# Performance work log

Hardware: AMD Instinct MI355X
Metric: run time of the kernel (lower is better)

The kernel has to match this reference:

```python
import jax, jax.numpy as jnp
import numpy as np

B, C, H, W = 8, 256, 64, 64
NH = 8
CM = 2048
EPS = 1e-5


def setup_inputs() -> dict:
    key = jax.random.key(0)
    ks = jax.random.split(key, 16)
    n = lambda k, s: (jax.random.normal(k, s, dtype=jnp.float32) * 0.02)
    return {
        'x': jax.random.normal(ks[0], (B, C, H, W), dtype=jnp.float32),
        'Wqkv': n(ks[1], (C, 3 * C)), 'bqkv': n(ks[2], (3 * C,)),
        'dw_w': n(ks[3], (C, 1, 3, 3)), 'dw_b': n(ks[4], (C,)),
        'Wproj': n(ks[5], (C, C)), 'bproj': n(ks[6], (C,)),
        'bn1_g': jnp.ones((C,), jnp.float32), 'bn1_b': jnp.zeros((C,), jnp.float32),
        'bn1_m': n(ks[7], (C,)), 'bn1_v': jax.random.uniform(ks[8], (C,), dtype=jnp.float32) + 0.5,
        'alpha1': jnp.ones((1,), jnp.float32),
        'Wfc1': n(ks[9], (C, CM)), 'bfc1': n(ks[10], (CM,)),
        'Wfc2': n(ks[11], (CM, C)), 'bfc2': n(ks[12], (C,)),
        'bn2_g': jnp.ones((C,), jnp.float32), 'bn2_b': jnp.zeros((C,), jnp.float32),
        'bn2_m': n(ks[13], (C,)), 'bn2_v': jax.random.uniform(ks[14], (C,), dtype=jnp.float32) + 0.5,
        'alpha2': jnp.ones((1,), jnp.float32),
    }


def _repbn(x, g, b, m, v, alpha):
    # eval-mode RepBN: BatchNorm1d with running stats over channel dim + alpha*x
    bn = (x - m) * jax.lax.rsqrt(v + EPS) * g + b
    return bn + alpha * x


def reference(x, Wqkv, bqkv, dw_w, dw_b, Wproj, bproj,
              bn1_g, bn1_b, bn1_m, bn1_v, alpha1,
              Wfc1, bfc1, Wfc2, bfc2,
              bn2_g, bn2_b, bn2_m, bn2_v, alpha2):
    b, c, h, w = x.shape
    n = h * w
    hd = c // NH
    scale = hd ** (-0.5)
    t = x.reshape(b, c, n).transpose(0, 2, 1)  # [B,N,C]

    # --- SimplifiedLinearAttention ---
    qkv = (t @ Wqkv + bqkv).reshape(b, n, 3, NH, hd).transpose(2, 0, 3, 1, 4)
    q, k, v = qkv[0], qkv[1], qkv[2]          # [B,H,N,hd]
    q = jax.nn.relu(q) * scale
    k = jax.nn.relu(k)
    ctx = jnp.einsum('bhnd,bhne->bhde', k, v)  # [B,H,hd,hd] small context
    out = jnp.einsum('bhnd,bhde->bhne', q, ctx)
    out = out.transpose(0, 2, 1, 3).reshape(b, n, c)
    img = out.transpose(0, 2, 1).reshape(b, c, h, w)
    img = jax.lax.conv_general_dilated(img, dw_w, (1, 1), 'SAME',
                                       feature_group_count=c)
    img = img + dw_b[None, :, None, None]
    out = img.reshape(b, c, n).transpose(0, 2, 1)
    out = out @ Wproj + bproj

    # residual + RepBN (eval branch of LinearNorm)
    t = _repbn(t + out, bn1_g, bn1_b, bn1_m, bn1_v, alpha1)

    # FFN (exact GELU as nn.GELU default)
    ff = jax.nn.gelu(t @ Wfc1 + bfc1, approximate=False) @ Wfc2 + bfc2
    t = _repbn(t + ff, bn2_g, bn2_b, bn2_m, bn2_v, alpha2)

    return t.transpose(0, 2, 1).reshape(b, c, h, w)
```

## Files before the change

### kernel.cpp

```cpp
#include <hip/hip_runtime.h>
#include <hip/hip_bf16.h>
#include <math.h>

constexpr int B_ = 8, C_ = 256, H_ = 64, W_ = 64;
constexpr int N_ = H_ * W_;
constexpr int NH_ = 8;
constexpr int CM_ = 2048;
constexpr int M_ = B_ * N_;
constexpr float EPS_ = 1e-5f;

typedef __bf16 bf16_t;
typedef bf16_t bf16x4 __attribute__((ext_vector_type(4)));
typedef bf16_t bf16x8 __attribute__((ext_vector_type(8)));
typedef float f32x4 __attribute__((ext_vector_type(4)));

__device__ inline bf16_t f2b(float f) {
    __hip_bfloat16 h = __float2bfloat16(f);
    return *reinterpret_cast<bf16_t*>(&h);
}
__device__ inline float b2f(bf16_t b) {
    unsigned short u = *reinterpret_cast<unsigned short*>(&b);
    unsigned int x = (unsigned int)u << 16;
    return *reinterpret_cast<float*>(&x);
}
__device__ inline unsigned pk2(float lo, float hi) {
    bf16_t l = f2b(lo), h = f2b(hi);
    unsigned short ls = *reinterpret_cast<unsigned short*>(&l);
    unsigned short hs = *reinterpret_cast<unsigned short*>(&h);
    return ((unsigned)hs << 16) | (unsigned)ls;
}
__device__ inline float gelu_ap(float y) {
    float u = y * (0.7978845608f + 0.0356774081f * y * y);
    float e = __expf(2.0f * u);
    return y - y * __builtin_amdgcn_rcpf(e + 1.0f);
}

#define GLOAD_LDS16(gptr, lptr)                                                     \
    __builtin_amdgcn_global_load_lds(                                               \
        (const __attribute__((address_space(1))) void*)(gptr),                      \
        (__attribute__((address_space(3))) void*)(lptr), 16, 0, 0)

__global__ __launch_bounds__(256)
void prep(const float* __restrict__ x, bf16_t* __restrict__ t_b,
          const float* __restrict__ Wqkv, bf16_t* __restrict__ WqkvT,
          const float* __restrict__ Wproj, bf16_t* __restrict__ WprojT,
          const float* __restrict__ Wfc1, bf16_t* __restrict__ Wfc1T,
          const float* __restrict__ Wfc2, bf16_t* __restrict__ Wfc2T) {
    __shared__ float tile[32][33];
    int id = blockIdx.x;
    int tx = threadIdx.x, ty = threadIdx.y;

    const float* src;
    bf16_t* dst;
    int K, N, k0, n0;

    if (id < 8192) {
        int b = id >> 10, rem = id & 1023;
        int nn = (rem & 127) * 32, cc = (rem >> 7) * 32;
#pragma unroll
        for (int i = ty; i < 32; i += 8)
            tile[i][tx] = x[(size_t)b * C_ * N_ + (size_t)(cc + i) * N_ + nn + tx];
        __syncthreads();
#pragma unroll
        for (int i = ty; i < 32; i += 8)
            t_b[(size_t)b * N_ * C_ + (size_t)(nn + i) * C_ + cc + tx] = f2b(tile[tx][i]);
        return;
    } else if (id < 8384) {
        int idw = id - 8192; K = C_; N = 768;
        n0 = (idw % 24) * 32; k0 = (idw / 24) * 32;
        src = Wqkv; dst = WqkvT;
    } else if (id < 8448) {
        int idw = id - 8384; K = C_; N = C_;
        n0 = (idw & 7) * 32; k0 = (idw >> 3) * 32;
        src = Wproj; dst = WprojT;
    } else if (id < 8960) {
        int idw = id - 8448; K = C_; N = CM_;
        n0 = (idw & 63) * 32; k0 = (idw >> 6) * 32;
        src = Wfc1; dst = Wfc1T;
    } else {
        int idw = id - 8960; K = CM_; N = C_;
        n0 = (idw & 7) * 32; k0 = (idw >> 3) * 32;
        src = Wfc2; dst = Wfc2T;
    }
#pragma unroll
    for (int i = ty; i < 32; i += 8)
        tile[i][tx] = src[(size_t)(k0 + i) * N + n0 + tx];
    __syncthreads();
#pragma unroll
    for (int i = ty; i < 32; i += 8)
        dst[(size_t)(n0 + i) * K + k0 + tx] = f2b(tile[tx][i]);
}

template <int EPI>
__global__ __launch_bounds__(256, 4)
void gemm_swp(const bf16_t* __restrict__ Wt, const bf16_t* __restrict__ Act,
              const float* __restrict__ bias, bf16_t* __restrict__ Cb,
              int M, int N, int K,
              const bf16_t* __restrict__ tres_b,
              const float* __restrict__ g, const float* __restrict__ bb,
              const float* __restrict__ mm, const float* __restrict__ vv,
              const float* __restrict__ alpha) {
    __shared__ bf16x8 ldsv[2048];
    char* lds = (char*)ldsv;

    int tid  = threadIdx.x;
    int lane = tid & 63;
    int w    = tid >> 6;
    int wi   = w >> 1, wj = w & 1;

    int nwg = gridDim.x * gridDim.y;
    int bid = blockIdx.y * gridDim.x + blockIdx.x;
    int swz = (bid & 7) * (nwg >> 3) + (bid >> 3);
    int bx = swz % gridDim.x, by = swz / gridDim.x;
    int bch = bx * 128, bm = by * 128;

    int rowl = lane & 15, kq = lane >> 4;

    f32x4 acc[4][4] = {};

    for (int k0 = 0; k0 < K; k0 += 64) {
#pragma unroll
        for (int j = 0; j < 4; ++j) {
            int jj = w * 4 + j;
            int msub = jj >> 1, kh = jj & 1;
            const bf16_t* gw = Wt + ((size_t)(bch + msub * 16 + rowl) * K + k0 + kh * 32 + kq * 8);
            GLOAD_LDS16(gw, lds + jj * 1024);
            const bf16_t* ga = Act + ((size_t)(bm + msub * 16 + rowl) * K + k0 + kh * 32 + kq * 8);
            GLOAD_LDS16(ga, lds + 16384 + jj * 1024);
        }
        __syncthreads();
#pragma unroll
        for (int ks = 0; ks < 2; ++ks) {
            bf16x8 wf[4], af[4];
#pragma unroll
            for (int i = 0; i < 4; ++i) wf[i] = ldsv[((wi * 4 + i) * 2 + ks) * 64 + lane];
#pragma unroll
            for (int j = 0; j < 4; ++j) af[j] = ldsv[1024 + ((wj * 4 + j) * 2 + ks) * 64 + lane];
#pragma unroll
            for (int i = 0; i < 4; ++i)
#pragma unroll
                for (int j = 0; j < 4; ++j)
                    acc[i][j] = __builtin_amdgcn_mfma_f32_16x16x32_bf16(wf[i], af[j], acc[i][j], 0, 0, 0);
        }
        __syncthreads();
    }

    float alpha_v = (EPI == 1) ? alpha[0] : 0.f;
#pragma unroll
    for (int i = 0; i < 4; ++i) {
        int ch = bch + wi * 64 + i * 16 + (lane >> 4) * 4;
        f32x4 b4 = *(const f32x4*)(bias + ch);
        f32x4 rs4, B4, m4;
        if (EPI == 1) {
            f32x4 g4 = *(const f32x4*)(g + ch);
            f32x4 v4 = *(const f32x4*)(vv + ch);
            B4 = *(const f32x4*)(bb + ch);
            m4 = *(const f32x4*)(mm + ch);
#pragma unroll
            for (int r = 0; r < 4; ++r) rs4[r] = rsqrtf(v4[r] + EPS_) * g4[r];
        }
#pragma unroll
        for (int j = 0; j < 4; ++j) {
            int m = bm + wj * 64 + j * 16 + (lane & 15);
            f32x4 a = acc[i][j];
            bf16_t ob[4];
            if (EPI == 4) {
#pragma unroll
                for (int r = 0; r < 4; ++r) ob[r] = f2b(a[r] + b4[r]);
            } else {
                bf16x4 t4 = *(const bf16x4*)(tres_b + (size_t)m * N + ch);
#pragma unroll
                for (int r = 0; r < 4; ++r) {
                    float z = b2f(t4[r]) + a[r] + b4[r];
                    ob[r] = f2b((z - m4[r]) * rs4[r] + B4[r] + alpha_v * z);
                }
            }
            *(bf16x4*)(Cb + (size_t)m * N + ch) = *(bf16x4*)ob;
        }
    }
}

__global__ __launch_bounds__(512, 4)
void ffn_fused(const bf16_t* __restrict__ Act, const bf16_t* __restrict__ W1t,
               const bf16_t* __restrict__ W2t,
               const float* __restrict__ bfc1, const float* __restrict__ bfc2,
               const float* __restrict__ g, const float* __restrict__ bb,
               const float* __restrict__ mm, const float* __restrict__ vv,
               const float* __restrict__ alpha, float* __restrict__ out) {
    __shared__ char lds[65536];
    bf16x8* ldsA = (bf16x8*)lds;

    const int tid = threadIdx.x;
    const int lane = tid & 63;
    const int w = tid >> 6;
    const int l15 = lane & 15;
    const int kq = lane >> 4;
    const int m0 = blockIdx.x * 64;

#pragma unroll
    for (int j = 0; j < 4; ++j) {
        int jj = w * 4 + j;
        int mblk = jj >> 3, ks = jj & 7;
        const bf16_t* src = Act + (size_t)(m0 + mblk * 16 + l15) * 256 + ks * 32 + kq * 8;
        GLOAD_LDS16(src, lds + jj * 1024);
    }
    __syncthreads();

    f32x4 acc2[2][4] = {};

    const int hrow = w * 16 + l15;
    const int ks2w = w >> 1;
    const int lane2 = l15 + (((2 * w + (kq >> 1)) & 3) << 4);
    const int hwoff = (kq & 1) << 3;
    const int chb = w * 32;

    bf16x8 w1f[8];
#pragma unroll
    for (int ks = 0; ks < 8; ++ks)
        w1f[ks] = *(const bf16x8*)(W1t + (size_t)hrow * 256 + ks * 32 + kq * 8);

    for (int c = 0; c < 16; ++c) {
        f32x4 acc1[4] = {};
#pragma unroll
        for (int ks = 0; ks < 8; ++ks)
#pragma unroll
            for (int mblk = 0; mblk < 4; ++mblk)
                acc1[mblk] = __builtin_amdgcn_mfma_f32_16x16x32_bf16(
                    w1f[ks], ldsA[(mblk * 8 + ks) * 64 + lane], acc1[mblk], 0, 0, 0);

        if (c + 1 < 16) {
#pragma unroll
            for (int ks = 0; ks < 8; ++ks)
                w1f[ks] = *(const bf16x8*)(W1t + (size_t)((c + 1) * 128 + hrow) * 256 + ks * 32 + kq * 8);
        }
        bf16x8 w2f[2][4];
#pragma unroll
        for (int cf = 0; cf < 2; ++cf)
#pragma unroll
            for (int ks2 = 0; ks2 < 4; ++ks2)
                w2f[cf][ks2] = *(const bf16x8*)(W2t + (size_t)(chb + cf * 16 + l15) * 2048 + c * 128 + ks2 * 32 + kq * 8);

        f32x4 b1 = *(const f32x4*)(bfc1 + c * 128 + w * 16 + kq * 4);
        char* hbase = lds + 32768 + (c & 1) * 16384;
#pragma unroll
        for (int mblk = 0; mblk < 4; ++mblk) {
            uint2 u2;
            u2.x = pk2(gelu_ap(acc1[mblk][0] + b1[0]), gelu_ap(acc1[mblk][1] + b1[1]));
            u2.y = pk2(gelu_ap(acc1[mblk][2] + b1[2]), gelu_ap(acc1[mblk][3] + b1[3]));
            *(uint2*)(hbase + (size_t)((mblk * 4 + ks2w) * 64 + lane2) * 16 + hwoff) = u2;
        }
        __syncthreads();

        bf16x8* ldsH = (bf16x8*)(lds + 32768 + (c & 1) * 16384);
#pragma unroll
        for (int mblk = 0; mblk < 4; ++mblk)
#pragma unroll
            for (int ks2 = 0; ks2 < 4; ++ks2) {
                bf16x8 hf = ldsH[(mblk * 4 + ks2) * 64 + lane];
                acc2[0][mblk] = __builtin_amdgcn_mfma_f32_16x16x32_bf16(hf, w2f[0][ks2], acc2[0][mblk], 0, 0, 0);
                acc2[1][mblk] = __builtin_amdgcn_mfma_f32_16x16x32_bf16(hf, w2f[1][ks2], acc2[1][mblk], 0, 0, 0);
            }
    }

    float alpha_v = alpha[0];
#pragma unroll
    for (int cf = 0; cf < 2; ++cf) {
        int ch = chb + cf * 16 + l15;
        float b2v = bfc2[ch];
        float rs = rsqrtf(vv[ch] + EPS_) * g[ch];
        float bbv = bb[ch], mv = mm[ch];
#pragma unroll
        for (int mblk = 0; mblk < 4; ++mblk) {
            int mbase = m0 + mblk * 16 + kq * 4;
            f32x4 o4;
#pragma unroll
            for (int r = 0; r < 4; ++r) {
                float z = b2f(Act[(size_t)(mbase + r) * 256 + ch]) + acc2[cf][mblk][r] + b2v;
                o4[r] = (z - mv) * rs + bbv + alpha_v * z;
            }
            int bi = mbase >> 12, ni = mbase & (N_ - 1);
            *(f32x4*)(out + ((size_t)bi * C_ + ch) * N_ + ni) = o4;
        }
    }
}

__global__ void transpose_b(const bf16_t* __restrict__ in_, bf16_t* __restrict__ outb) {
    __shared__ float tile[32][33];
    int b  = blockIdx.z;
    int n0 = blockIdx.x * 32;
    int c0 = blockIdx.y * 32;
    int tx = threadIdx.x, ty = threadIdx.y;
#pragma unroll
    for (int i = ty; i < 32; i += 8)
        tile[i][tx] = b2f(in_[(size_t)b * C_ * N_ + (size_t)(c0 + i) * N_ + n0 + tx]);
    __syncthreads();
#pragma unroll
    for (int i = ty; i < 32; i += 8)
        outb[(size_t)b * N_ * C_ + (size_t)(n0 + i) * C_ + c0 + tx] = f2b(tile[tx][i]);
}

__global__ void ctx_partial(const bf16_t* __restrict__ qkv, float* __restrict__ ctxp) {
    __shared__ float kb[64][40];
    __shared__ float vb[64][40];
    int seg = blockIdx.x;
    int bh  = blockIdx.y;
    int b = bh >> 3, h = bh & 7;
    int tid = threadIdx.x;
    int d  = tid >> 3;
    int e0 = (tid & 7) * 4;
    int lrow = tid >> 2, lcol = (tid & 3) * 8;
    float acc[4] = {0.f, 0.f, 0.f, 0.f};
    const size_t base = (size_t)b * N_ * 768 + h * 32;
    for (int n0 = seg * 512; n0 < seg * 512 + 512; n0 += 64) {
        size_t ra = base + (size_t)(n0 + lrow) * 768 + lcol;
        bf16x8 kv8 = *(const bf16x8*)(qkv + ra + 256);
        bf16x8 vv8 = *(const bf16x8*)(qkv + ra + 512);
#pragma unroll
        for (int j = 0; j < 8; ++j) {
            kb[lrow][lcol + j] = b2f(kv8[j]);
            vb[lrow][lcol + j] = b2f(vv8[j]);
        }
        __syncthreads();
#pragma unroll
        for (int nl = 0; nl < 64; ++nl) {
            float kv = fmaxf(kb[nl][d], 0.f);
#pragma unroll
            for (int j = 0; j < 4; ++j)
                acc[j] = fmaf(kv, vb[nl][e0 + j], acc[j]);
        }
        __syncthreads();
    }
    float* o = ctxp + ((size_t)seg * 64 + bh) * 1024 + d * 32 + e0;
#pragma unroll
    for (int j = 0; j < 4; ++j) o[j] = acc[j];
}

__global__ void ctx_reduce(const float* __restrict__ ctxp, float* __restrict__ ctx) {
    int idx = blockIdx.x * 256 + threadIdx.x;
    float s = 0.f;
#pragma unroll
    for (int seg = 0; seg < 8; ++seg) s += ctxp[(size_t)seg * 65536 + idx];
    ctx[idx] = s;
}

__global__ void attn_out(const bf16_t* __restrict__ qkv, const float* __restrict__ ctx,
                         bf16_t* __restrict__ img) {
    __shared__ float qb[64][33];
    __shared__ float cs[32][32];
    int n0 = blockIdx.x * 64;
    int bh = blockIdx.y;
    int b = bh >> 3, h = bh & 7;
    int tid = threadIdx.x;
    const float scale = 0.17677669529663687f;
    {
        float4 vv = ((const float4*)(ctx + (size_t)bh * 1024))[tid];
        ((float4*)&cs[0][0])[tid] = vv;
    }
    const size_t base = (size_t)b * N_ * 768 + h * 32;
    int lrow = tid >> 2, lcol = (tid & 3) * 8;
    {
        bf16x8 q8 = *(const bf16x8*)(qkv + base + (size_t)(n0 + lrow) * 768 + lcol);
#pragma unroll
        for (int j = 0; j < 8; ++j)
            qb[lrow][lcol + j] = fmaxf(b2f(q8[j]), 0.f) * scale;
    }
    __syncthreads();
    int nl = tid & 63, ebase = tid >> 6;
    bf16_t* outp = img + ((size_t)b * C_ + h * 32) * N_ + n0 + nl;
#pragma unroll
    for (int p = 0; p < 8; ++p) {
        int e = ebase + p * 4;
        float s = 0.f;
#pragma unroll
        for (int dd = 0; dd < 32; ++dd)
            s = fmaf(qb[nl][dd], cs[dd][e], s);
        outp[(size_t)e * N_] = f2b(s);
    }
}

__global__ __launch_bounds__(256)
void dwconv3x3(const bf16_t* __restrict__ img, const float* __restrict__ w,
               const float* __restrict__ bias, bf16_t* __restrict__ out) {
    __shared__ float sp[64][65];
    int bc = blockIdx.x;
    int c  = bc & 255;
    int tid = threadIdx.x;
    const bf16_t* ip = img + (size_t)bc * N_;
#pragma unroll
    for (int l = 0; l < 2; ++l) {
        int flat = (tid + l * 256) * 8;
        int row = flat >> 6, col = flat & 63;
        bf16x8 v8 = *(const bf16x8*)(ip + flat);
#pragma unroll
        for (int j = 0; j < 8; ++j) sp[row][col + j] = b2f(v8[j]);
    }
    float wv[9];
#pragma unroll
    for (int j = 0; j < 9; ++j) wv[j] = w[c * 9 + j];
    float bv = bias[c];
    __syncthreads();

    int y = tid >> 2, x0 = (tid & 3) * 16;
    float o[16];
#pragma unroll
    for (int i = 0; i < 16; ++i) o[i] = bv;
#pragma unroll
    for (int dy = -1; dy <= 1; ++dy) {
        int yy = y + dy;
        if (yy < 0 || yy > 63) continue;
#pragma unroll
        for (int dx = -1; dx <= 1; ++dx) {
            float wgt = wv[(dy + 1) * 3 + dx + 1];
#pragma unroll
            for (int i = 0; i < 16; ++i) {
                int xx = x0 + i + dx;
                float val = (xx < 0 || xx > 63) ? 0.f : sp[yy][xx];
                o[i] = fmaf(wgt, val, o[i]);
            }
        }
    }
    bf16_t ob[16];
#pragma unroll
    for (int i = 0; i < 16; ++i) ob[i] = f2b(o[i]);
    *(bf16x8*)(out + (size_t)bc * N_ + y * 64 + x0)     = *(bf16x8*)&ob[0];
    *(bf16x8*)(out + (size_t)bc * N_ + y * 64 + x0 + 8) = *(bf16x8*)&ob[8];
}

extern "C" void kernel_launch(void* const* d_in, const int* in_sizes, int n_in,
                              void* d_out, int out_size, void* d_ws, size_t ws_size,
                              hipStream_t stream) {
    const float* x     = (const float*)d_in[0];
    const float* Wqkv  = (const float*)d_in[1];
    const float* bqkv  = (const float*)d_in[2];
    const float* dw_w  = (const float*)d_in[3];
    const float* dw_b  = (const float*)d_in[4];
    const float* Wproj = (const float*)d_in[5];
    const float* bproj = (const float*)d_in[6];
    const float* bn1_g = (const float*)d_in[7];
    const float* bn1_b = (const float*)d_in[8];
    const float* bn1_m = (const float*)d_in[9];
    const float* bn1_v = (const float*)d_in[10];
    const float* alpha1= (const float*)d_in[11];
    const float* Wfc1  = (const float*)d_in[12];
    const float* bfc1  = (const float*)d_in[13];
    const float* Wfc2  = (const float*)d_in[14];
    const float* bfc2  = (const float*)d_in[15];
    const float* bn2_g = (const float*)d_in[16];
    const float* bn2_b = (const float*)d_in[17];
    const float* bn2_m = (const float*)d_in[18];
    const float* bn2_v = (const float*)d_in[19];
    const float* alpha2= (const float*)d_in[20];
    float* out = (float*)d_out;

    char* ws = (char*)d_ws;
    bf16_t* t_b2    = (bf16_t*)(ws);
    bf16_t* WqkvT   = (bf16_t*)(ws + 16777216);
    bf16_t* WprojT  = (bf16_t*)(ws + 17170432);
    bf16_t* Wfc1T   = (bf16_t*)(ws + 17301504);
    bf16_t* Wfc2T   = (bf16_t*)(ws + 18350080);
    float*  ctxp    = (float*)(ws + 19398656);
    float*  ctx     = (float*)(ws + 21495808);
    bf16_t* t_b     = (bf16_t*)(ws + 21757952);
    bf16_t* qkv_b   = (bf16_t*)(ws + 38535168);
    bf16_t* img_b   = (bf16_t*)(ws + 88866816);
    bf16_t* conv_b  = (bf16_t*)(ws + 105644032);
    bf16_t* convT_b = (bf16_t*)(ws + 122421248);

    prep<<<9472, dim3(32, 8), 0, stream>>>(x, t_b, Wqkv, WqkvT, Wproj, WprojT,
                                           Wfc1, Wfc1T, Wfc2, Wfc2T);

    gemm_swp<4><<<dim3(768 / 128, M_ / 128), 256, 0, stream>>>(
        WqkvT, t_b, bqkv, qkv_b, M_, 768, C_,
        nullptr, nullptr, nullptr, nullptr, nullptr, nullptr);

    ctx_partial<<<dim3(8, B_ * NH_), 256, 0, stream>>>(qkv_b, ctxp);
    ctx_reduce<<<256, 256, 0, stream>>>(ctxp, ctx);

    attn_out<<<dim3(N_ / 64, B_ * NH_), 256, 0, stream>>>(qkv_b, ctx, img_b);

    dwconv3x3<<<B_ * C_, 256, 0, stream>>>(img_b, dw_w, dw_b, conv_b);

    transpose_b<<<dim3(N_ / 32, C_ / 32, B_), dim3(32, 8), 0, stream>>>(conv_b, convT_b);

    gemm_swp<1><<<dim3(C_ / 128, M_ / 128), 256, 0, stream>>>(
        WprojT, convT_b, bproj, t_b2, M_, C_, C_,
        t_b, bn1_g, bn1_b, bn1_m, bn1_v, alpha1);

    ffn_fused<<<M_ / 64, 512, 0, stream>>>(
        t_b2, Wfc1T, Wfc2T, bfc1, bfc2,
        bn2_g, bn2_b, bn2_m, bn2_v, alpha2, out);
}
```

Measured before the change: 296.6 us.

## Switch FFN first GEMM to 32x32x16 MFMA with split accumulators and priority hints

Reworks the first FFN GEMM in the fused FFN kernel to use 32x32x16 bf16 MFMA instructions. Each wave now computes a 32x32 tile split across two independent accumulator chains, and the activation tile in LDS is re-laid out to match. W1 is loaded per chunk in two halves instead of prefetched one chunk ahead, and s_setprio is raised around the MFMA sections. The intent is to use larger MFMA tiles and hide dependency latency, at the cost of losing the cross-iteration W1 prefetch and changing register pressure.

```diff
diff --git a/kernel.cpp b/kernel.cpp
--- a/kernel.cpp
+++ b/kernel.cpp
@@ -13,6 +13,7 @@
 typedef bf16_t bf16x4 __attribute__((ext_vector_type(4)));
 typedef bf16_t bf16x8 __attribute__((ext_vector_type(8)));
 typedef float f32x4 __attribute__((ext_vector_type(4)));
+typedef float f32x16 __attribute__((ext_vector_type(16)));
 
 __device__ inline bf16_t f2b(float f) {
     __hip_bfloat16 h = __float2bfloat16(f);
@@ -194,45 +195,62 @@
     const int lane = tid & 63;
     const int w = tid >> 6;
     const int l15 = lane & 15;
+    const int l31 = lane & 31;
+    const int h5 = lane >> 5;
     const int kq = lane >> 4;
     const int m0 = blockIdx.x * 64;
 
 #pragma unroll
     for (int j = 0; j < 4; ++j) {
         int jj = w * 4 + j;
-        int mblk = jj >> 3, ks = jj & 7;
-        const bf16_t* src = Act + (size_t)(m0 + mblk * 16 + l15) * 256 + ks * 32 + kq * 8;
+        int mh = jj >> 4, ks = jj & 15;
+        const bf16_t* src = Act + (size_t)(m0 + mh * 32 + l31) * 256 + ks * 16 + h5 * 8;
         GLOAD_LDS16(src, lds + jj * 1024);
     }
     __syncthreads();
 
     f32x4 acc2[2][4] = {};
 
-    const int hrow = w * 16 + l15;
-    const int ks2w = w >> 1;
-    const int lane2 = l15 + (((2 * w + (kq >> 1)) & 3) << 4);
-    const int hwoff = (kq & 1) << 3;
+    const int wh = w >> 1;
+    const int wm = w & 1;
+    const int mblkw = wm * 2 + (l31 >> 4);
     const int chb = w * 32;
 
-    bf16x8 w1f[8];
-#pragma unroll
-    for (int ks = 0; ks < 8; ++ks)
-        w1f[ks] = *(const bf16x8*)(W1t + (size_t)hrow * 256 + ks * 32 + kq * 8);
-
     for (int c = 0; c < 16; ++c) {
-        f32x4 acc1[4] = {};
-#pragma unroll
-        for (int ks = 0; ks < 8; ++ks)
-#pragma unroll
-            for (int mblk = 0; mblk < 4; ++mblk)
-                acc1[mblk] = __builtin_amdgcn_mfma_f32_16x16x32_bf16(
-                    w1f[ks], ldsA[(mblk * 8 + ks) * 64 + lane], acc1[mblk], 0, 0, 0);
-
-        if (c + 1 < 16) {
+        const bf16_t* w1p = W1t + (size_t)(c * 128 + wh * 32 + l31) * 256 + h5 * 8;
+        f32x16 a1a = (f32x16)0.f, a1b = (f32x16)0.f;
+        {
+            bf16x8 wl[8];
 #pragma unroll
             for (int ks = 0; ks < 8; ++ks)
-                w1f[ks] = *(const bf16x8*)(W1t + (size_t)((c + 1) * 128 + hrow) * 256 + ks * 32 + kq * 8);
-        }
+                wl[ks] = *(const bf16x8*)(w1p + ks * 16);
+            __builtin_amdgcn_s_setprio(1);
+#pragma unroll
+            for (int ks = 0; ks < 4; ++ks) {
+                a1a = __builtin_amdgcn_mfma_f32_32x32x16_bf16(
+                    wl[2 * ks], ldsA[(wm * 16 + 2 * ks) * 64 + lane], a1a, 0, 0, 0);
+                a1b = __builtin_amdgcn_mfma_f32_32x32x16_bf16(
+                    wl[2 * ks + 1], ldsA[(wm * 16 + 2 * ks + 1) * 64 + lane], a1b, 0, 0, 0);
+            }
+            __builtin_amdgcn_s_setprio(0);
+        }
+        {
+            bf16x8 wl[8];
+#pragma unroll
+            for (int ks = 0; ks < 8; ++ks)
+                wl[ks] = *(const bf16x8*)(w1p + (ks + 8) * 16);
+            __builtin_amdgcn_s_setprio(1);
+#pragma unroll
+            for (int ks = 0; ks < 4; ++ks) {
+                a1a = __builtin_amdgcn_mfma_f32_32x32x16_bf16(
+                    wl[2 * ks], ldsA[(wm * 16 + 8 + 2 * ks) * 64 + lane], a1a, 0, 0, 0);
+                a1b = __builtin_amdgcn_mfma_f32_32x32x16_bf16(
+                    wl[2 * ks + 1], ldsA[(wm * 16 + 8 + 2 * ks + 1) * 64 + lane], a1b, 0, 0, 0);
+            }
+            __builtin_amdgcn_s_setprio(0);
+        }
+        f32x16 acc1 = a1a + a1b;
+
         bf16x8 w2f[2][4];
 #pragma unroll
         for (int cf = 0; cf < 2; ++cf)
@@ -240,18 +258,19 @@
             for (int ks2 = 0; ks2 < 4; ++ks2)
                 w2f[cf][ks2] = *(const bf16x8*)(W2t + (size_t)(chb + cf * 16 + l15) * 2048 + c * 128 + ks2 * 32 + kq * 8);
 
-        f32x4 b1 = *(const f32x4*)(bfc1 + c * 128 + w * 16 + kq * 4);
         char* hbase = lds + 32768 + (c & 1) * 16384;
 #pragma unroll
-        for (int mblk = 0; mblk < 4; ++mblk) {
+        for (int rr = 0; rr < 4; ++rr) {
+            f32x4 b1 = *(const f32x4*)(bfc1 + c * 128 + wh * 32 + 8 * rr + 4 * h5);
             uint2 u2;
-            u2.x = pk2(gelu_ap(acc1[mblk][0] + b1[0]), gelu_ap(acc1[mblk][1] + b1[1]));
-            u2.y = pk2(gelu_ap(acc1[mblk][2] + b1[2]), gelu_ap(acc1[mblk][3] + b1[3]));
-            *(uint2*)(hbase + (size_t)((mblk * 4 + ks2w) * 64 + lane2) * 16 + hwoff) = u2;
+            u2.x = pk2(gelu_ap(acc1[4 * rr + 0] + b1[0]), gelu_ap(acc1[4 * rr + 1] + b1[1]));
+            u2.y = pk2(gelu_ap(acc1[4 * rr + 2] + b1[2]), gelu_ap(acc1[4 * rr + 3] + b1[3]));
+            *(uint2*)(hbase + (size_t)(((mblkw * 4 + wh) * 64) + (l15 + (rr << 4))) * 16 + h5 * 8) = u2;
         }
         __syncthreads();
 
         bf16x8* ldsH = (bf16x8*)(lds + 32768 + (c & 1) * 16384);
+        __builtin_amdgcn_s_setprio(1);
 #pragma unroll
         for (int mblk = 0; mblk < 4; ++mblk)
 #pragma unroll
@@ -260,6 +279,7 @@
                 acc2[0][mblk] = __builtin_amdgcn_mfma_f32_16x16x32_bf16(hf, w2f[0][ks2], acc2[0][mblk], 0, 0, 0);
                 acc2[1][mblk] = __builtin_amdgcn_mfma_f32_16x16x32_bf16(hf, w2f[1][ks2], acc2[1][mblk], 0, 0, 0);
             }
+        __builtin_amdgcn_s_setprio(0);
     }
 
     float alpha_v = alpha[0];
```

Result: slower. 389.6 us (+31.4%).

## Fuse ctx reduction into attn_out and dwconv with transpose

Applied to the files above, without the earlier changes.

Removes the ctx_reduce kernel by having each attn_out block sum the eight partial context segments itself. It also replaces the separate dwconv and transpose kernels with one kernel. That kernel computes the 3x3 depthwise conv for one row and 32 channels, then writes the result channel-last through a shared-memory tile. This cuts two kernel launches and a full intermediate round-trip through global memory. The cost is redundant partial-sum reads in attn_out and reloading of three input rows per output row, which roughly triples conv input traffic.

```diff
diff --git a/kernel.cpp b/kernel.cpp
--- a/kernel.cpp
+++ b/kernel.cpp
@@ -284,21 +284,6 @@
     }
 }
 
-__global__ void transpose_b(const bf16_t* __restrict__ in_, bf16_t* __restrict__ outb) {
-    __shared__ float tile[32][33];
-    int b  = blockIdx.z;
-    int n0 = blockIdx.x * 32;
-    int c0 = blockIdx.y * 32;
-    int tx = threadIdx.x, ty = threadIdx.y;
-#pragma unroll
-    for (int i = ty; i < 32; i += 8)
-        tile[i][tx] = b2f(in_[(size_t)b * C_ * N_ + (size_t)(c0 + i) * N_ + n0 + tx]);
-    __syncthreads();
-#pragma unroll
-    for (int i = ty; i < 32; i += 8)
-        outb[(size_t)b * N_ * C_ + (size_t)(n0 + i) * C_ + c0 + tx] = f2b(tile[tx][i]);
-}
-
 __global__ void ctx_partial(const bf16_t* __restrict__ qkv, float* __restrict__ ctxp) {
     __shared__ float kb[64][40];
     __shared__ float vb[64][40];
@@ -335,15 +320,7 @@
     for (int j = 0; j < 4; ++j) o[j] = acc[j];
 }
 
-__global__ void ctx_reduce(const float* __restrict__ ctxp, float* __restrict__ ctx) {
-    int idx = blockIdx.x * 256 + threadIdx.x;
-    float s = 0.f;
-#pragma unroll
-    for (int seg = 0; seg < 8; ++seg) s += ctxp[(size_t)seg * 65536 + idx];
-    ctx[idx] = s;
-}
-
-__global__ void attn_out(const bf16_t* __restrict__ qkv, const float* __restrict__ ctx,
+__global__ void attn_out(const bf16_t* __restrict__ qkv, const float* __restrict__ ctxp,
                          bf16_t* __restrict__ img) {
     __shared__ float qb[64][33];
     __shared__ float cs[32][32];
@@ -353,8 +330,13 @@
     int tid = threadIdx.x;
     const float scale = 0.17677669529663687f;
     {
-        float4 vv = ((const float4*)(ctx + (size_t)bh * 1024))[tid];
-        ((float4*)&cs[0][0])[tid] = vv;
+        f32x4 vv = (f32x4)0.f;
+#pragma unroll
+        for (int seg = 0; seg < 8; ++seg) {
+            f32x4 t = ((const f32x4*)(ctxp + ((size_t)seg * 64 + bh) * 1024))[tid];
+            vv = vv + t;
+        }
+        ((f32x4*)&cs[0][0])[tid] = vv;
     }
     const size_t base = (size_t)b * N_ * 768 + h * 32;
     int lrow = tid >> 2, lcol = (tid & 3) * 8;
@@ -379,20 +361,27 @@
 }
 
 __global__ __launch_bounds__(256)
-void dwconv3x3(const bf16_t* __restrict__ img, const float* __restrict__ w,
-               const float* __restrict__ bias, bf16_t* __restrict__ out) {
-    __shared__ float sp[64][65];
-    int bc = blockIdx.x;
-    int c  = bc & 255;
+void dwconvT(const bf16_t* __restrict__ img, const float* __restrict__ w,
+             const float* __restrict__ bias, bf16_t* __restrict__ outb) {
+    __shared__ float spf[3][32][66];
+    __shared__ float otile[64][33];
+    int id = blockIdx.x;
+    int cg = id & 7, y = (id >> 3) & 63, b = id >> 9;
     int tid = threadIdx.x;
-    const bf16_t* ip = img + (size_t)bc * N_;
-#pragma unroll
-    for (int l = 0; l < 2; ++l) {
-        int flat = (tid + l * 256) * 8;
-        int row = flat >> 6, col = flat & 63;
-        bf16x8 v8 = *(const bf16x8*)(ip + flat);
-#pragma unroll
-        for (int j = 0; j < 8; ++j) sp[row][col + j] = b2f(v8[j]);
+    int c_l = tid >> 3, xg = tid & 7;
+    int c = cg * 32 + c_l;
+    const bf16_t* ip = img + (size_t)(b * C_ + c) * N_;
+#pragma unroll
+    for (int dy = 0; dy < 3; ++dy) {
+        int yy = y + dy - 1;
+        if (yy < 0 || yy > 63) {
+#pragma unroll
+            for (int j = 0; j < 8; ++j) spf[dy][c_l][xg * 8 + j] = 0.f;
+        } else {
+            bf16x8 v8 = *(const bf16x8*)(ip + yy * 64 + xg * 8);
+#pragma unroll
+            for (int j = 0; j < 8; ++j) spf[dy][c_l][xg * 8 + j] = b2f(v8[j]);
+        }
     }
     float wv[9];
 #pragma unroll
@@ -400,30 +389,30 @@
     float bv = bias[c];
     __syncthreads();
 
-    int y = tid >> 2, x0 = (tid & 3) * 16;
-    float o[16];
-#pragma unroll
-    for (int i = 0; i < 16; ++i) o[i] = bv;
-#pragma unroll
-    for (int dy = -1; dy <= 1; ++dy) {
-        int yy = y + dy;
-        if (yy < 0 || yy > 63) continue;
+    float o[8];
+#pragma unroll
+    for (int i = 0; i < 8; ++i) o[i] = bv;
+#pragma unroll
+    for (int dy = 0; dy < 3; ++dy)
 #pragma unroll
         for (int dx = -1; dx <= 1; ++dx) {
-            float wgt = wv[(dy + 1) * 3 + dx + 1];
-#pragma unroll
-            for (int i = 0; i < 16; ++i) {
-                int xx = x0 + i + dx;
-                float val = (xx < 0 || xx > 63) ? 0.f : sp[yy][xx];
+            float wgt = wv[dy * 3 + dx + 1];
+#pragma unroll
+            for (int i = 0; i < 8; ++i) {
+                int xx = xg * 8 + i + dx;
+                float val = (xx < 0 || xx > 63) ? 0.f : spf[dy][c_l][xx];
                 o[i] = fmaf(wgt, val, o[i]);
             }
         }
-    }
-    bf16_t ob[16];
-#pragma unroll
-    for (int i = 0; i < 16; ++i) ob[i] = f2b(o[i]);
-    *(bf16x8*)(out + (size_t)bc * N_ + y * 64 + x0)     = *(bf16x8*)&ob[0];
-    *(bf16x8*)(out + (size_t)bc * N_ + y * 64 + x0 + 8) = *(bf16x8*)&ob[8];
+#pragma unroll
+    for (int i = 0; i < 8; ++i) otile[xg * 8 + i][c_l] = o[i];
+    __syncthreads();
+
+    int x_o = tid >> 2, cq = tid & 3;
+    bf16_t ob[8];
+#pragma unroll
+    for (int j = 0; j < 8; ++j) ob[j] = f2b(otile[x_o][cq * 8 + j]);
+    *(bf16x8*)(outb + ((size_t)b * N_ + y * 64 + x_o) * 256 + cg * 32 + cq * 8) = *(bf16x8*)&ob[0];
 }
 
 extern "C" void kernel_launch(void* const* d_in, const int* in_sizes, int n_in,
@@ -459,11 +448,9 @@
     bf16_t* Wfc1T   = (bf16_t*)(ws + 17301504);
     bf16_t* Wfc2T   = (bf16_t*)(ws + 18350080);
     float*  ctxp    = (float*)(ws + 19398656);
-    float*  ctx     = (float*)(ws + 21495808);
     bf16_t* t_b     = (bf16_t*)(ws + 21757952);
     bf16_t* qkv_b   = (bf16_t*)(ws + 38535168);
     bf16_t* img_b   = (bf16_t*)(ws + 88866816);
-    bf16_t* conv_b  = (bf16_t*)(ws + 105644032);
     bf16_t* convT_b = (bf16_t*)(ws + 122421248);
 
     prep<<<9472, dim3(32, 8), 0, stream>>>(x, t_b, Wqkv, WqkvT, Wproj, WprojT,
@@ -474,13 +461,10 @@
         nullptr, nullptr, nullptr, nullptr, nullptr, nullptr);
 
     ctx_partial<<<dim3(8, B_ * NH_), 256, 0, stream>>>(qkv_b, ctxp);
-    ctx_reduce<<<256, 256, 0, stream>>>(ctxp, ctx);
-
-    attn_out<<<dim3(N_ / 64, B_ * NH_), 256, 0, stream>>>(qkv_b, ctx, img_b);
-
-    dwconv3x3<<<B_ * C_, 256, 0, stream>>>(img_b, dw_w, dw_b, conv_b);
-
-    transpose_b<<<dim3(N_ / 32, C_ / 32, B_), dim3(32, 8), 0, stream>>>(conv_b, convT_b);
+
+    attn_out<<<dim3(N_ / 64, B_ * NH_), 256, 0, stream>>>(qkv_b, ctxp, img_b);
+
+    dwconvT<<<B_ * 64 * 8, 256, 0, stream>>>(img_b, dw_w, dw_b, convT_b);
 
     gemm_swp<1><<<dim3(C_ / 128, M_ / 128), 256, 0, stream>>>(
         WprojT, convT_b, bproj, t_b2, M_, C_, C_,
```

Result: faster. 286.9 us, median of 4 (-3.3%).
